# Optimization experiments

Hardware: AMD Instinct MI355X
Metric: run time of the kernel (lower is better)

The kernel has to match this reference:

```python
import jax, jax.numpy as jnp
import numpy as np

B, S, I, H, L1, O = 128, 1024, 256, 512, 256, 64

def _xavier(key, shape):
    fan_in, fan_out = shape[-2] if len(shape) > 1 else shape[-1], shape[-1]
    limit = float(np.sqrt(6.0 / (fan_in + fan_out)))
    return jax.random.uniform(key, shape, jnp.float32, -limit, limit)

def setup_inputs() -> dict:
    key = jax.random.key(0)
    ks = jax.random.split(key, 20)
    d = {"X": jax.random.normal(ks[0], (B, S, I), jnp.float32)}
    names = [("W_xi", (I, H)), ("W_hi", (H, H)), ("b_i", (1, H)),
             ("W_xf", (I, H)), ("W_hf", (H, H)), ("b_f", (1, H)),
             ("W_xo", (I, H)), ("W_ho", (H, H)), ("b_o", (1, H)),
             ("W_xc", (I, H)), ("W_hc", (H, H)), ("b_c", (1, H)),
             ("W_o1", (H, L1)), ("b_o1", (1, L1)), ("W_o2", (L1, O)), ("b_o2", (1, O))]
    for k, (n, shp) in zip(ks[1:], names):
        d[n] = _xavier(k, shp)
    return d

def reference(X, W_xi, W_hi, b_i, W_xf, W_hf, b_f, W_xo, W_ho, b_o, W_xc, W_hc, b_c, W_o1, b_o1, W_o2, b_o2):
    batch = X.shape[0]
    hid = W_hi.shape[0]
    # Precompute all input projections in one big GEMM: [B,S,4H]
    Wx = jnp.concatenate([W_xi, W_xf, W_xo, W_xc], axis=1)
    pre = jnp.einsum('bsi,ig->bsg', X, Wx)  # [B,S,4H]
    pre = jnp.transpose(pre, (1, 0, 2))     # [S,B,4H] for scan

    def step(carry, p):
        Hs, Cs = carry
        pi, pf, po, pc = jnp.split(p, 4, axis=-1)
        Ig = jax.nn.sigmoid(pi + Hs @ W_hi + b_i)
        Fg = jax.nn.sigmoid(pf + Hs @ W_hf + b_f)
        Og = jax.nn.sigmoid(po + Hs @ W_ho + b_o)
        Ct = jnp.tanh(pc + Hs @ W_hc + b_c)
        Cn = Fg * Cs + Ig * Ct
        # NOTE: original module uses tanh(C) + O (addition), not O * tanh(C)
        Hn = jnp.tanh(Cn) + Og
        return (Hn, Cn), None

    H0 = jnp.zeros((batch, hid), X.dtype)
    C0 = jnp.zeros((batch, hid), X.dtype)
    (Hf, Cf), _ = jax.lax.scan(step, (H0, C0), pre)
    # Output head: only the final timestep's output is returned by the loop
    h1 = jax.nn.relu(Hf @ W_o1 + b_o1)
    output = jax.nn.softmax(h1 @ W_o2 + b_o2, axis=1)
    return output, Hf, Cf
```

## Files before the change

### kernel.cpp

```cpp
#include <hip/hip_runtime.h>

#define B_   128
#define S_   1024
#define I_   256
#define H_   512
#define L1_  256
#define O_   64

#define NGRP 8
#define WGPG 32
#define MB   16
#define NH   16
#define NCOL 64
#define SX   8
#define SH   16

#define HB_UINTS_PER_BUF 32768

typedef __attribute__((ext_vector_type(8))) short short8;
typedef __attribute__((ext_vector_type(4))) float f4;
typedef __attribute__((ext_vector_type(4))) unsigned u32x4;

__device__ __forceinline__ unsigned short f2bf(float x) {
  unsigned u = __builtin_bit_cast(unsigned, x);
  u += 0x7FFFu + ((u >> 16) & 1u);
  return (unsigned short)(u >> 16);
}

__device__ __forceinline__ f4 mfma_bf16(short8 a, short8 b, f4 c) {
  asm("v_mfma_f32_16x16x32_bf16 %0, %1, %2, %0" : "+v"(c) : "v"(a), "v"(b));
  return c;
}

__global__ __launch_bounds__(256, 1)
void lstm_rec(const float* __restrict__ X,
              const float* __restrict__ Wxi, const float* __restrict__ Whi, const float* __restrict__ bi,
              const float* __restrict__ Wxf, const float* __restrict__ Whf, const float* __restrict__ bfp,
              const float* __restrict__ Wxo, const float* __restrict__ Who, const float* __restrict__ bop,
              const float* __restrict__ Wxc, const float* __restrict__ Whc, const float* __restrict__ bcp,
              float* __restrict__ out, unsigned* __restrict__ flags,
              unsigned* __restrict__ xslots, unsigned* __restrict__ Hbuf)
{
  __shared__ unsigned short WhF[4][SH][64][8];
  __shared__ unsigned short WxF[4][SX][64][8];
  __shared__ unsigned short AsH[SH][64][8];
  __shared__ float Ps[MB][NCOL];
  __shared__ float bias_s[NCOL];
  __shared__ int go_s;
  __shared__ int mode_s;

  const int tid  = threadIdx.x;
  const int lane = tid & 63;
  const int wv   = tid >> 6;
  const int g    = blockIdx.x & 7;
  const int jg   = blockIdx.x >> 3;
  const int j0   = jg * NH;
  const int b0   = g * MB;

  unsigned xcc;
  asm volatile("s_getreg_b32 %0, hwreg(HW_REG_XCC_ID)" : "=s"(xcc));
  xcc &= 15u;
  if (tid == 0)
    __hip_atomic_store(xslots + g * 32 + jg, xcc + 1u,
                       __ATOMIC_RELAXED, __HIP_MEMORY_SCOPE_AGENT);

  const int idxA = tid, idxB = 256 + tid;
  const int sA = idxA >> 6, posA = idxA & 63;
  const int sB = idxB >> 6, posB = idxB & 63;
  const int offA = (sA * 64 + posA) * 8;
  const int offB = (sB * 64 + posB) * 8;
  const float* bpa = X + (size_t)(b0 + (posA & 15)) * S_ * I_ + (sA * 32 + (posA >> 4) * 8);
  const float* bpb = X + (size_t)(b0 + (posB & 15)) * S_ * I_ + (sB * 32 + (posB >> 4) * 8);
  float4 ra0 = *(const float4*)(bpa);
  float4 ra1 = *(const float4*)(bpa + 4);
  float4 rb0 = *(const float4*)(bpb);
  float4 rb1 = *(const float4*)(bpb + 4);

  const float* Whg[4] = {Whi, Whf, Who, Whc};
  const float* Wxg[4] = {Wxi, Wxf, Wxo, Wxc};
  const float* bg[4]  = {bi, bfp, bop, bcp};

  for (int gate = 0; gate < 4; ++gate) {
    const float* Wp = Whg[gate];
    for (int it = 0; it < 32; ++it) {
      int idx = it * 256 + tid;
      int k = idx >> 4, c = idx & 15;
      WhF[gate][k >> 5][((k & 31) >> 3) * 16 + c][k & 7] = f2bf(Wp[(size_t)k * H_ + j0 + c]);
    }
    const float* Xp = Wxg[gate];
    for (int it = 0; it < 16; ++it) {
      int idx = it * 256 + tid;
      int k = idx >> 4, c = idx & 15;
      WxF[gate][k >> 5][((k & 31) >> 3) * 16 + c][k & 7] = f2bf(Xp[(size_t)k * H_ + j0 + c]);
    }
  }
  if (tid < NCOL) bias_s[tid] = bg[tid >> 4][j0 + (tid & 15)];
  if (tid == 0) go_s = 0;
  __syncthreads();

  short8 wx[SX], wh[SH];
  #pragma unroll
  for (int s = 0; s < SX; ++s) wx[s] = *(const short8*)&WxF[wv][s][lane][0];
  #pragma unroll
  for (int s = 0; s < SH; ++s) wh[s] = *(const short8*)&WhF[wv][s][lane][0];

  if (wv == 0) {
    unsigned v;
    for (;;) {
      v = __hip_atomic_load(xslots + g * 32 + (lane & 31),
                            __ATOMIC_RELAXED, __HIP_MEMORY_SCOPE_AGENT);
      if (__all((int)(v != 0u))) break;
      __builtin_amdgcn_s_sleep(1);
    }
    unsigned f0 = (unsigned)__shfl((int)v, 0, 64);
    int same = __all((int)(v == f0));
    if (lane == 0) mode_s = same;
  }
  __syncthreads();
  const bool l2m = (mode_s != 0);

  unsigned short* axbase = &WxF[0][0][0][0];
  const int AXSTRIDE = SX * 64 * 8;
  {
    union { unsigned short us[8]; u32x4 v; } pk;
    pk.us[0]=f2bf(ra0.x); pk.us[1]=f2bf(ra0.y); pk.us[2]=f2bf(ra0.z); pk.us[3]=f2bf(ra0.w);
    pk.us[4]=f2bf(ra1.x); pk.us[5]=f2bf(ra1.y); pk.us[6]=f2bf(ra1.z); pk.us[7]=f2bf(ra1.w);
    *(u32x4*)(axbase + offA) = pk.v;
    pk.us[0]=f2bf(rb0.x); pk.us[1]=f2bf(rb0.y); pk.us[2]=f2bf(rb0.z); pk.us[3]=f2bf(rb0.w);
    pk.us[4]=f2bf(rb1.x); pk.us[5]=f2bf(rb1.y); pk.us[6]=f2bf(rb1.z); pk.us[7]=f2bf(rb1.w);
    *(u32x4*)(axbase + offB) = pk.v;
  }
  __syncthreads();

  float Creg = 0.f;
  const int pb = tid >> 4;
  const int ph = tid & 15;
  unsigned* myflags = flags + g * 32;

  for (int t = 0; t < S_; ++t) {
    const bool last = (t == S_ - 1);

    unsigned fpre = 0u;
    const unsigned* fp0 = myflags + (lane & 31);
    if (t > 0 && wv == 0)
      asm volatile("global_load_dword %0, %1, off sc0 sc1"
                   : "+v"(fpre) : "v"(fp0) : "memory");

    float bv = bias_s[wv * 16 + (lane & 15)];
    f4 acc = {bv, bv, bv, bv};
    asm("s_nop 1" : "+v"(acc));
    const unsigned short* ax = axbase + (t & 1) * AXSTRIDE;
    #pragma unroll
    for (int s = 0; s < SX; ++s) {
      short8 a = *(const short8*)(ax + (s * 64 + lane) * 8);
      acc = mfma_bf16(a, wx[s], acc);
    }

    if (t > 0) {
      if (wv == 0) {
        asm volatile("s_waitcnt vmcnt(0)" : "+v"(fpre) :: "memory");
        __builtin_amdgcn_sched_barrier(0);
        if (!__all((int)(fpre >= (unsigned)t))) {
          for (;;) {
            unsigned v = __hip_atomic_load(fp0, __ATOMIC_RELAXED, __HIP_MEMORY_SCOPE_AGENT);
            if (__all((int)(v >= (unsigned)t))) break;
            __builtin_amdgcn_s_sleep(1);
          }
        }
        if (lane == 0) *(volatile int*)&go_s = (int)t;
      } else {
        while (*(volatile int*)&go_s < (int)t) __builtin_amdgcn_s_sleep(1);
      }
      const u32x4* gp = (const u32x4*)(Hbuf + (size_t)(t & 1) * HB_UINTS_PER_BUF + g * 4096);
      u32x4 r0, r1, r2, r3;
      if (l2m) {
        asm volatile(
          "global_load_dwordx4 %0, %4, off sc0\n\t"
          "global_load_dwordx4 %1, %5, off sc0\n\t"
          "global_load_dwordx4 %2, %6, off sc0\n\t"
          "global_load_dwordx4 %3, %7, off sc0\n\t"
          "s_waitcnt vmcnt(0)"
          : "=&v"(r0), "=&v"(r1), "=&v"(r2), "=&v"(r3)
          : "v"(gp + tid), "v"(gp + tid + 256), "v"(gp + tid + 512), "v"(gp + tid + 768)
          : "memory");
      } else {
        asm volatile(
          "global_load_dwordx4 %0, %4, off sc0 sc1\n\t"
          "global_load_dwordx4 %1, %5, off sc0 sc1\n\t"
          "global_load_dwordx4 %2, %6, off sc0 sc1\n\t"
          "global_load_dwordx4 %3, %7, off sc0 sc1\n\t"
          "s_waitcnt vmcnt(0)"
          : "=&v"(r0), "=&v"(r1), "=&v"(r2), "=&v"(r3)
          : "v"(gp + tid), "v"(gp + tid + 256), "v"(gp + tid + 512), "v"(gp + tid + 768)
          : "memory");
      }
      u32x4* lp = (u32x4*)&AsH[0][0][0];
      lp[tid]       = r0;
      lp[tid + 256] = r1;
      lp[tid + 512] = r2;
      lp[tid + 768] = r3;
    }
    __syncthreads();

    if (!last) {
      const float* pa = bpa + (size_t)(t + 1) * I_;
      const float* pb2 = bpb + (size_t)(t + 1) * I_;
      ra0 = *(const float4*)(pa);
      ra1 = *(const float4*)(pa + 4);
      rb0 = *(const float4*)(pb2);
      rb1 = *(const float4*)(pb2 + 4);
    }

    if (t > 0) {
      #pragma unroll
      for (int s = 0; s < SH; ++s) {
        short8 a = *(const short8*)&AsH[s][lane][0];
        acc = mfma_bf16(a, wh[s], acc);
      }
    }
    asm("s_nop 7\n\ts_nop 7" : "+v"(acc));
    {
      int col = wv * 16 + (lane & 15);
      int r0i = (lane >> 4) * 4;
      Ps[r0i + 0][col] = acc[0];
      Ps[r0i + 1][col] = acc[1];
      Ps[r0i + 2][col] = acc[2];
      Ps[r0i + 3][col] = acc[3];
    }
    __syncthreads();

    {
      float pi = Ps[pb][ph];
      float pf = Ps[pb][16 + ph];
      float po = Ps[pb][32 + ph];
      float pc = Ps[pb][48 + ph];
      float Ig = 1.f / (1.f + __expf(-pi));
      float Fg = 1.f / (1.f + __expf(-pf));
      float Og = 1.f / (1.f + __expf(-po));
      float Ct = 1.f - 2.f / (__expf(2.f * pc) + 1.f);
      float Cn = Fg * Creg + Ig * Ct;
      Creg = Cn;
      float Hn = (1.f - 2.f / (__expf(2.f * Cn) + 1.f)) + Og;
      if (!last) {
        unsigned hb = f2bf(Hn);
        unsigned other = (unsigned)__shfl_xor((int)hb, 1, 64);
        if ((ph & 1) == 0) {
          unsigned packed = hb | (other << 16);
          int sl = jg >> 1;
          int pos = ((jg & 1) * 2 + (ph >> 3)) * 16 + pb;
          unsigned* dst = Hbuf + (size_t)((t + 1) & 1) * HB_UINTS_PER_BUF + g * 4096
                        + (sl * 64 + pos) * 4 + ((ph & 7) >> 1);
          if (l2m)
            asm volatile("global_store_dword %0, %1, off sc0" :: "v"(dst), "v"(packed) : "memory");
          else
            asm volatile("global_store_dword %0, %1, off sc0 sc1" :: "v"(dst), "v"(packed) : "memory");
        }
      } else {
        out[B_ * O_ + (size_t)(b0 + pb) * H_ + j0 + ph] = Hn;
        out[B_ * O_ + B_ * H_ + (size_t)(b0 + pb) * H_ + j0 + ph] = Cn;
      }
    }
    if (!last) {
      unsigned short* axw = axbase + ((t + 1) & 1) * AXSTRIDE;
      union { unsigned short us[8]; u32x4 v; } pk;
      pk.us[0]=f2bf(ra0.x); pk.us[1]=f2bf(ra0.y); pk.us[2]=f2bf(ra0.z); pk.us[3]=f2bf(ra0.w);
      pk.us[4]=f2bf(ra1.x); pk.us[5]=f2bf(ra1.y); pk.us[6]=f2bf(ra1.z); pk.us[7]=f2bf(ra1.w);
      *(u32x4*)(axw + offA) = pk.v;
      pk.us[0]=f2bf(rb0.x); pk.us[1]=f2bf(rb0.y); pk.us[2]=f2bf(rb0.z); pk.us[3]=f2bf(rb0.w);
      pk.us[4]=f2bf(rb1.x); pk.us[5]=f2bf(rb1.y); pk.us[6]=f2bf(rb1.z); pk.us[7]=f2bf(rb1.w);
      *(u32x4*)(axw + offB) = pk.v;

      __syncthreads();
      if (tid == 0)
        __hip_atomic_store(myflags + jg, (unsigned)(t + 1),
                           __ATOMIC_RELAXED, __HIP_MEMORY_SCOPE_AGENT);
    }
  }
}

__global__ __launch_bounds__(256, 1)
void lstm_head(const float* __restrict__ Hf,
               const float* __restrict__ Wo1, const float* __restrict__ bo1,
               const float* __restrict__ Wo2, const float* __restrict__ bo2,
               float* __restrict__ outp)
{
  __shared__ float hf[H_];
  __shared__ float h1[L1_];
  const int tid = threadIdx.x;
  const int b = blockIdx.x;
  hf[tid]       = Hf[(size_t)b * H_ + tid];
  hf[tid + 256] = Hf[(size_t)b * H_ + tid + 256];
  __syncthreads();
  float a = bo1[tid];
  #pragma unroll 8
  for (int k = 0; k < H_; ++k) a = fmaf(hf[k], Wo1[(size_t)k * L1_ + tid], a);
  h1[tid] = fmaxf(a, 0.f);
  __syncthreads();
  if (tid < O_) {
    float l = bo2[tid];
    #pragma unroll 8
    for (int j = 0; j < L1_; ++j) l = fmaf(h1[j], Wo2[(size_t)j * O_ + tid], l);
    float m = l;
    #pragma unroll
    for (int off = 32; off > 0; off >>= 1) m = fmaxf(m, __shfl_xor(m, off, 64));
    float e = __expf(l - m);
    float ssum = e;
    #pragma unroll
    for (int off = 32; off > 0; off >>= 1) ssum += __shfl_xor(ssum, off, 64);
    outp[(size_t)b * O_ + tid] = e / ssum;
  }
}

extern "C" void kernel_launch(void* const* d_in, const int* in_sizes, int n_in,
                              void* d_out, int out_size, void* d_ws, size_t ws_size,
                              hipStream_t stream) {
  (void)in_sizes; (void)n_in; (void)out_size; (void)ws_size;
  const float* X   = (const float*)d_in[0];
  const float* Wxi = (const float*)d_in[1];
  const float* Whi = (const float*)d_in[2];
  const float* bi  = (const float*)d_in[3];
  const float* Wxf = (const float*)d_in[4];
  const float* Whf = (const float*)d_in[5];
  const float* bfv = (const float*)d_in[6];
  const float* Wxo = (const float*)d_in[7];
  const float* Who = (const float*)d_in[8];
  const float* bo  = (const float*)d_in[9];
  const float* Wxc = (const float*)d_in[10];
  const float* Whc = (const float*)d_in[11];
  const float* bc  = (const float*)d_in[12];
  const float* Wo1 = (const float*)d_in[13];
  const float* bo1 = (const float*)d_in[14];
  const float* Wo2 = (const float*)d_in[15];
  const float* bo2 = (const float*)d_in[16];
  float* out = (float*)d_out;

  unsigned* flags  = (unsigned*)d_ws;
  unsigned* xslots = (unsigned*)((char*)d_ws + 1024);
  unsigned* Hbuf   = (unsigned*)((char*)d_ws + 2048);

  hipMemsetAsync(d_ws, 0, 2048, stream);
  hipLaunchKernelGGL(lstm_rec, dim3(NGRP * WGPG), dim3(256), 0, stream,
                     X, Wxi, Whi, bi, Wxf, Whf, bfv, Wxo, Who, bo, Wxc, Whc, bc,
                     out, flags, xslots, Hbuf);
  hipLaunchKernelGGL(lstm_head, dim3(B_), dim3(256), 0, stream,
                     out + B_ * O_, Wo1, bo1, Wo2, bo2, out);
}
```

Measured before the change: 2.292 ms.

## Remap gate columns per wave to drop cross-wave barrier and flag broadcast

Rearranges the weight fragments so each wave holds all four gates for four hidden columns, letting each wave apply the LSTM cell from its own accumulators through a small per-wave LDS scratch instead of a block-wide barrier. Every wave now polls the progress flags itself, removing the LDS go-flag handoff from wave 0. The change also splits the MFMA accumulation into two independent chains to shorten dependency latency and uses packed bf16 convert instructions for staging X and H. In exchange, flag-polling traffic to global memory rises by four times per block, and the added accumulator adds register pressure.

```diff
diff --git a/kernel.cpp b/kernel.cpp
--- a/kernel.cpp
+++ b/kernel.cpp
@@ -11,7 +11,6 @@
 #define WGPG 32
 #define MB   16
 #define NH   16
-#define NCOL 64
 #define SX   8
 #define SH   16
 
@@ -30,6 +29,16 @@
 __device__ __forceinline__ f4 mfma_bf16(short8 a, short8 b, f4 c) {
   asm("v_mfma_f32_16x16x32_bf16 %0, %1, %2, %0" : "+v"(c) : "v"(a), "v"(b));
   return c;
+}
+
+__device__ __forceinline__ void stage_chunk(unsigned short* dst, f4 a, f4 b) {
+  unsigned d0, d1, d2, d3;
+  asm("v_cvt_pk_bf16_f32 %0, %1, %2" : "=v"(d0) : "v"(a[0]), "v"(a[1]));
+  asm("v_cvt_pk_bf16_f32 %0, %1, %2" : "=v"(d1) : "v"(a[2]), "v"(a[3]));
+  asm("v_cvt_pk_bf16_f32 %0, %1, %2" : "=v"(d2) : "v"(b[0]), "v"(b[1]));
+  asm("v_cvt_pk_bf16_f32 %0, %1, %2" : "=v"(d3) : "v"(b[2]), "v"(b[3]));
+  u32x4 v = {d0, d1, d2, d3};
+  *(u32x4*)dst = v;
 }
 
 __global__ __launch_bounds__(256, 1)
@@ -44,9 +53,7 @@
   __shared__ unsigned short WhF[4][SH][64][8];
   __shared__ unsigned short WxF[4][SX][64][8];
   __shared__ unsigned short AsH[SH][64][8];
-  __shared__ float Ps[MB][NCOL];
-  __shared__ float bias_s[NCOL];
-  __shared__ int go_s;
+  __shared__ float Psw[4][16][20];
   __shared__ int mode_s;
 
   const int tid  = threadIdx.x;
@@ -71,14 +78,14 @@
   const int offB = (sB * 64 + posB) * 8;
   const float* bpa = X + (size_t)(b0 + (posA & 15)) * S_ * I_ + (sA * 32 + (posA >> 4) * 8);
   const float* bpb = X + (size_t)(b0 + (posB & 15)) * S_ * I_ + (sB * 32 + (posB >> 4) * 8);
-  float4 ra0 = *(const float4*)(bpa);
-  float4 ra1 = *(const float4*)(bpa + 4);
-  float4 rb0 = *(const float4*)(bpb);
-  float4 rb1 = *(const float4*)(bpb + 4);
+  f4 ra0 = *(const f4*)(bpa);
+  f4 ra1 = *(const f4*)(bpa + 4);
+  f4 rb0 = *(const f4*)(bpb);
+  f4 rb1 = *(const f4*)(bpb + 4);
 
   const float* Whg[4] = {Whi, Whf, Who, Whc};
   const float* Wxg[4] = {Wxi, Wxf, Wxo, Wxc};
-  const float* bg[4]  = {bi, bfp, bop, bcp};
+  const float* bgp[4] = {bi, bfp, bop, bcp};
 
   for (int gate = 0; gate < 4; ++gate) {
     const float* Wp = Whg[gate];
@@ -94,15 +101,21 @@
       WxF[gate][k >> 5][((k & 31) >> 3) * 16 + c][k & 7] = f2bf(Xp[(size_t)k * H_ + j0 + c]);
     }
   }
-  if (tid < NCOL) bias_s[tid] = bg[tid >> 4][j0 + (tid & 15)];
-  if (tid == 0) go_s = 0;
-  __syncthreads();
-
+  if (tid == 0) mode_s = 0;
+  __syncthreads();
+
+  const int colL  = lane & 15;
+  const int rgrpL = lane >> 4;
+  const int gateL = colL >> 2;
+  const int ccL   = colL & 3;
   short8 wx[SX], wh[SH];
   #pragma unroll
-  for (int s = 0; s < SX; ++s) wx[s] = *(const short8*)&WxF[wv][s][lane][0];
+  for (int s = 0; s < SX; ++s)
+    wx[s] = *(const short8*)&WxF[gateL][s][rgrpL * 16 + wv * 4 + ccL][0];
   #pragma unroll
-  for (int s = 0; s < SH; ++s) wh[s] = *(const short8*)&WhF[wv][s][lane][0];
+  for (int s = 0; s < SH; ++s)
+    wh[s] = *(const short8*)&WhF[gateL][s][rgrpL * 16 + wv * 4 + ccL][0];
+  const float bv = bgp[gateL][j0 + wv * 4 + ccL];
 
   if (wv == 0) {
     unsigned v;
@@ -121,55 +134,48 @@
 
   unsigned short* axbase = &WxF[0][0][0][0];
   const int AXSTRIDE = SX * 64 * 8;
-  {
-    union { unsigned short us[8]; u32x4 v; } pk;
-    pk.us[0]=f2bf(ra0.x); pk.us[1]=f2bf(ra0.y); pk.us[2]=f2bf(ra0.z); pk.us[3]=f2bf(ra0.w);
-    pk.us[4]=f2bf(ra1.x); pk.us[5]=f2bf(ra1.y); pk.us[6]=f2bf(ra1.z); pk.us[7]=f2bf(ra1.w);
-    *(u32x4*)(axbase + offA) = pk.v;
-    pk.us[0]=f2bf(rb0.x); pk.us[1]=f2bf(rb0.y); pk.us[2]=f2bf(rb0.z); pk.us[3]=f2bf(rb0.w);
-    pk.us[4]=f2bf(rb1.x); pk.us[5]=f2bf(rb1.y); pk.us[6]=f2bf(rb1.z); pk.us[7]=f2bf(rb1.w);
-    *(u32x4*)(axbase + offB) = pk.v;
-  }
+  stage_chunk(axbase + offA, ra0, ra1);
+  stage_chunk(axbase + offB, rb0, rb1);
   __syncthreads();
 
   float Creg = 0.f;
-  const int pb = tid >> 4;
-  const int ph = tid & 15;
+  const int rowG = lane >> 2;
+  const int cG   = lane & 3;
+  const int jG   = j0 + wv * 4 + cG;
+  const int dwH  = (((jG >> 5) * 64) + ((jG >> 3) & 3) * 16 + rowG) * 4 + ((jG & 7) >> 1);
+
   unsigned* myflags = flags + g * 32;
+  const unsigned* fp0 = myflags + (lane & 31);
 
   for (int t = 0; t < S_; ++t) {
     const bool last = (t == S_ - 1);
 
     unsigned fpre = 0u;
-    const unsigned* fp0 = myflags + (lane & 31);
-    if (t > 0 && wv == 0)
+    if (t > 0)
       asm volatile("global_load_dword %0, %1, off sc0 sc1"
                    : "+v"(fpre) : "v"(fp0) : "memory");
 
-    float bv = bias_s[wv * 16 + (lane & 15)];
-    f4 acc = {bv, bv, bv, bv};
-    asm("s_nop 1" : "+v"(acc));
+    f4 acc0 = {bv, bv, bv, bv};
+    f4 acc1 = {0.f, 0.f, 0.f, 0.f};
+    asm("s_nop 1" : "+v"(acc0));
+    asm("s_nop 1" : "+v"(acc1));
     const unsigned short* ax = axbase + (t & 1) * AXSTRIDE;
     #pragma unroll
     for (int s = 0; s < SX; ++s) {
       short8 a = *(const short8*)(ax + (s * 64 + lane) * 8);
-      acc = mfma_bf16(a, wx[s], acc);
+      if (s & 1) acc1 = mfma_bf16(a, wx[s], acc1);
+      else       acc0 = mfma_bf16(a, wx[s], acc0);
     }
 
     if (t > 0) {
-      if (wv == 0) {
-        asm volatile("s_waitcnt vmcnt(0)" : "+v"(fpre) :: "memory");
-        __builtin_amdgcn_sched_barrier(0);
-        if (!__all((int)(fpre >= (unsigned)t))) {
-          for (;;) {
-            unsigned v = __hip_atomic_load(fp0, __ATOMIC_RELAXED, __HIP_MEMORY_SCOPE_AGENT);
-            if (__all((int)(v >= (unsigned)t))) break;
-            __builtin_amdgcn_s_sleep(1);
-          }
+      asm volatile("s_waitcnt vmcnt(0)" : "+v"(fpre) :: "memory");
+      __builtin_amdgcn_sched_barrier(0);
+      if (!__all((int)(fpre >= (unsigned)t))) {
+        for (;;) {
+          unsigned v = __hip_atomic_load(fp0, __ATOMIC_RELAXED, __HIP_MEMORY_SCOPE_AGENT);
+          if (__all((int)(v >= (unsigned)t))) break;
+          __builtin_amdgcn_s_sleep(1);
         }
-        if (lane == 0) *(volatile int*)&go_s = (int)t;
-      } else {
-        while (*(volatile int*)&go_s < (int)t) __builtin_amdgcn_s_sleep(1);
       }
       const u32x4* gp = (const u32x4*)(Hbuf + (size_t)(t & 1) * HB_UINTS_PER_BUF + g * 4096);
       u32x4 r0, r1, r2, r3;
@@ -203,77 +209,64 @@
     __syncthreads();
 
     if (!last) {
-      const float* pa = bpa + (size_t)(t + 1) * I_;
+      const float* pa  = bpa + (size_t)(t + 1) * I_;
       const float* pb2 = bpb + (size_t)(t + 1) * I_;
-      ra0 = *(const float4*)(pa);
-      ra1 = *(const float4*)(pa + 4);
-      rb0 = *(const float4*)(pb2);
-      rb1 = *(const float4*)(pb2 + 4);
+      ra0 = *(const f4*)(pa);
+      ra1 = *(const f4*)(pa + 4);
+      rb0 = *(const f4*)(pb2);
+      rb1 = *(const f4*)(pb2 + 4);
     }
 
     if (t > 0) {
       #pragma unroll
       for (int s = 0; s < SH; ++s) {
         short8 a = *(const short8*)&AsH[s][lane][0];
-        acc = mfma_bf16(a, wh[s], acc);
+        if (s & 1) acc1 = mfma_bf16(a, wh[s], acc1);
+        else       acc0 = mfma_bf16(a, wh[s], acc0);
       }
     }
-    asm("s_nop 7\n\ts_nop 7" : "+v"(acc));
-    {
-      int col = wv * 16 + (lane & 15);
-      int r0i = (lane >> 4) * 4;
-      Ps[r0i + 0][col] = acc[0];
-      Ps[r0i + 1][col] = acc[1];
-      Ps[r0i + 2][col] = acc[2];
-      Ps[r0i + 3][col] = acc[3];
-    }
-    __syncthreads();
-
-    {
-      float pi = Ps[pb][ph];
-      float pf = Ps[pb][16 + ph];
-      float po = Ps[pb][32 + ph];
-      float pc = Ps[pb][48 + ph];
-      float Ig = 1.f / (1.f + __expf(-pi));
-      float Fg = 1.f / (1.f + __expf(-pf));
-      float Og = 1.f / (1.f + __expf(-po));
-      float Ct = 1.f - 2.f / (__expf(2.f * pc) + 1.f);
-      float Cn = Fg * Creg + Ig * Ct;
-      Creg = Cn;
-      float Hn = (1.f - 2.f / (__expf(2.f * Cn) + 1.f)) + Og;
-      if (!last) {
-        unsigned hb = f2bf(Hn);
-        unsigned other = (unsigned)__shfl_xor((int)hb, 1, 64);
-        if ((ph & 1) == 0) {
-          unsigned packed = hb | (other << 16);
-          int sl = jg >> 1;
-          int pos = ((jg & 1) * 2 + (ph >> 3)) * 16 + pb;
-          unsigned* dst = Hbuf + (size_t)((t + 1) & 1) * HB_UINTS_PER_BUF + g * 4096
-                        + (sl * 64 + pos) * 4 + ((ph & 7) >> 1);
-          if (l2m)
-            asm volatile("global_store_dword %0, %1, off sc0" :: "v"(dst), "v"(packed) : "memory");
-          else
-            asm volatile("global_store_dword %0, %1, off sc0 sc1" :: "v"(dst), "v"(packed) : "memory");
-        }
-      } else {
-        out[B_ * O_ + (size_t)(b0 + pb) * H_ + j0 + ph] = Hn;
-        out[B_ * O_ + B_ * H_ + (size_t)(b0 + pb) * H_ + j0 + ph] = Cn;
-      }
-    }
+    asm("s_nop 7" : "+v"(acc0));
+    asm("s_nop 7" : "+v"(acc1));
+    f4 accs = {acc0[0] + acc1[0], acc0[1] + acc1[1], acc0[2] + acc1[2], acc0[3] + acc1[3]};
+
+    *(f4*)&Psw[wv][colL][rgrpL * 4] = accs;
+    asm volatile("s_waitcnt lgkmcnt(0)" ::: "memory");
+    __builtin_amdgcn_sched_barrier(0);
+    float pi = Psw[wv][cG][rowG];
+    float pf = Psw[wv][4 + cG][rowG];
+    float po = Psw[wv][8 + cG][rowG];
+    float pc = Psw[wv][12 + cG][rowG];
+
+    float Ig = 1.f / (1.f + __expf(-pi));
+    float Fg = 1.f / (1.f + __expf(-pf));
+    float Og = 1.f / (1.f + __expf(-po));
+    float Ct = 1.f - 2.f / (__expf(2.f * pc) + 1.f);
+    float Cn = Fg * Creg + Ig * Ct;
+    Creg = Cn;
+    float Hn = (1.f - 2.f / (__expf(2.f * Cn) + 1.f)) + Og;
+
     if (!last) {
       unsigned short* axw = axbase + ((t + 1) & 1) * AXSTRIDE;
-      union { unsigned short us[8]; u32x4 v; } pk;
-      pk.us[0]=f2bf(ra0.x); pk.us[1]=f2bf(ra0.y); pk.us[2]=f2bf(ra0.z); pk.us[3]=f2bf(ra0.w);
-      pk.us[4]=f2bf(ra1.x); pk.us[5]=f2bf(ra1.y); pk.us[6]=f2bf(ra1.z); pk.us[7]=f2bf(ra1.w);
-      *(u32x4*)(axw + offA) = pk.v;
-      pk.us[0]=f2bf(rb0.x); pk.us[1]=f2bf(rb0.y); pk.us[2]=f2bf(rb0.z); pk.us[3]=f2bf(rb0.w);
-      pk.us[4]=f2bf(rb1.x); pk.us[5]=f2bf(rb1.y); pk.us[6]=f2bf(rb1.z); pk.us[7]=f2bf(rb1.w);
-      *(u32x4*)(axw + offB) = pk.v;
-
+      stage_chunk(axw + offA, ra0, ra1);
+      stage_chunk(axw + offB, rb0, rb1);
+
+      float Hp = __shfl_xor(Hn, 1, 64);
+      if ((cG & 1) == 0) {
+        unsigned packed;
+        asm("v_cvt_pk_bf16_f32 %0, %1, %2" : "=v"(packed) : "v"(Hn), "v"(Hp));
+        unsigned* dst = Hbuf + (size_t)((t + 1) & 1) * HB_UINTS_PER_BUF + g * 4096 + dwH;
+        if (l2m)
+          asm volatile("global_store_dword %0, %1, off sc0" :: "v"(dst), "v"(packed) : "memory");
+        else
+          asm volatile("global_store_dword %0, %1, off sc0 sc1" :: "v"(dst), "v"(packed) : "memory");
+      }
       __syncthreads();
       if (tid == 0)
         __hip_atomic_store(myflags + jg, (unsigned)(t + 1),
                            __ATOMIC_RELAXED, __HIP_MEMORY_SCOPE_AGENT);
+    } else {
+      out[B_ * O_ + (size_t)(b0 + rowG) * H_ + jG] = Hn;
+      out[B_ * O_ + B_ * H_ + (size_t)(b0 + rowG) * H_ + jG] = Cn;
     }
   }
 }
@@ -338,7 +331,7 @@
   unsigned* xslots = (unsigned*)((char*)d_ws + 1024);
   unsigned* Hbuf   = (unsigned*)((char*)d_ws + 2048);
 
-  hipMemsetAsync(d_ws, 0, 2048, stream);
+  (void)hipMemsetAsync(d_ws, 0, 2048, stream);
   hipLaunchKernelGGL(lstm_rec, dim3(NGRP * WGPG), dim3(256), 0, stream,
                      X, Wxi, Whi, bi, Wxf, Whf, bfv, Wxo, Who, bo, Wxc, Whc, bc,
                      out, flags, xslots, Hbuf);
```

After: 2.164 ms. -5.6%, faster.
